# Optimization experiments

Hardware: AMD Instinct MI355X
Metric: run time of the kernel (lower is better)

## Reference

```python
import jax, jax.numpy as jnp
import numpy as np
from jax import lax

H_HID, W_HID = 8, 12
N_PAIR = H_HID * W_HID   # 96
NF = 32                  # mlp_nfilters
C_FEAT = 512 + 2         # phi_im channels + (x,y) coords


def _conv_relu(x, w, b):
    # 3x3 conv, stride 1, SAME padding (SingleConvBlock), then ReLU
    y = lax.conv_general_dilated(x, w, (1, 1), 'SAME',
                                 dimension_numbers=('NCHW', 'OIHW', 'NCHW'))
    return jax.nn.relu(y + b[None, :, None, None])


def _maxpool2(x):
    return lax.reduce_window(x, -jnp.inf, lax.max, (1, 1, 2, 2), (1, 1, 2, 2), 'VALID')


def setup_inputs() -> dict:
    key = jax.random.key(0)
    ks = jax.random.split(key, 16)
    d = {}
    d['x'] = jax.random.normal(ks[0], (4, 3, 64, 96), jnp.float32)
    d['sen_embed'] = jax.random.normal(ks[1], (4, 384), jnp.float32)

    def p(k, shape, fan_in):
        return (jax.random.normal(k, shape, jnp.float32) / np.float32(np.sqrt(fan_in)))

    d['enc1_w'] = p(ks[2], (64, 3, 3, 3), 3 * 9);      d['enc1_b'] = p(ks[3], (64,), 64)
    d['enc2_w'] = p(ks[4], (128, 64, 3, 3), 64 * 9);   d['enc2_b'] = p(ks[5], (128,), 128)
    d['enc3_w'] = p(ks[6], (256, 128, 3, 3), 128 * 9); d['enc3_b'] = p(ks[7], (256,), 256)
    d['enc4_w'] = p(ks[8], (512, 256, 3, 3), 256 * 9); d['enc4_b'] = p(ks[9], (512,), 512)
    d['g1_w'] = p(ks[10], (1412, 256), 1412);          d['g1_b'] = p(ks[11], (256,), 256)
    d['g2_w'] = p(ks[12], (256, 256), 256);            d['g2_b'] = p(ks[13], (256,), 256)
    d['g3_w'] = p(ks[14], (256, N_PAIR * NF), 256);    d['g3_b'] = p(ks[15], (N_PAIR * NF,), N_PAIR * NF)
    return d


def _forward(x, sen_embed, enc1_w, enc1_b, enc2_w, enc2_b, enc3_w, enc3_b,
             enc4_w, enc4_b, g1_w, g1_b, g2_w, g2_b, g3_w, g3_b):
    # ---- conv encoder ----
    e1 = _conv_relu(x, enc1_w, enc1_b)                     # [B,64,64,96]
    e2 = _conv_relu(_maxpool2(e1), enc2_w, enc2_b)         # [B,128,32,48]
    e3 = _conv_relu(_maxpool2(e2), enc3_w, enc3_b)         # [B,256,16,24]
    phi_im = _conv_relu(_maxpool2(e3), enc4_w, enc4_b)     # [B,512,8,12]
    B = phi_im.shape[0]

    # ---- coordinate grid (matches torch.meshgrid default 'ij' then reshape) ----
    xc = jnp.linspace(-1.0, 1.0, W_HID, dtype=phi_im.dtype)
    yc = jnp.linspace(-1.0, 1.0, H_HID, dtype=phi_im.dtype)
    xg, yg = jnp.meshgrid(xc, yc, indexing='ij')           # each [12,8]
    coord = jnp.stack([xg.reshape(H_HID, W_HID), yg.reshape(H_HID, W_HID)], axis=0)
    coord = jnp.broadcast_to(coord[None], (B, 2, H_HID, W_HID))

    # per-location features F: [B, n_pair, 514]
    F = jnp.concatenate([phi_im, coord], axis=1).reshape(B, C_FEAT, N_PAIR).transpose(0, 2, 1)

    # ---- all-pairs relation network ----
    # pair feature at (a,c) = concat(F[c], F[a], sen_embed); exploit linearity of first
    # Linear to avoid materializing the [B,n,n,1412] concat tensor (same math).
    A, Bm, Cm = g1_w[:C_FEAT], g1_w[C_FEAT:2 * C_FEAT], g1_w[2 * C_FEAT:]
    u = F @ A                                # i-part,  [B,n,256]
    v = F @ Bm                               # j-part,  [B,n,256]
    ws = sen_embed @ Cm + g1_b               # sentence part, [B,256]
    h1 = jax.nn.relu(u[:, None, :, :] + v[:, :, None, :] + ws[:, None, None, :])  # [B,n,n,256]
    h2 = jax.nn.relu(h1 @ g2_w + g2_b)                                           # [B,n,n,256]
    out = jax.nn.relu(h2 @ g3_w + g3_b)                                          # [B,n,n,3072]

    # sum over all n_pair^2 pairs, reshape to feature map [B,32,8,12]
    phi = out.sum(axis=(1, 2)).reshape(B, NF, H_HID, W_HID)
    return phi


def reference(x, sen_embed, enc1_w, enc1_b, enc2_w, enc2_b, enc3_w, enc3_b,
              enc4_w, enc4_b, g1_w, g1_b, g2_w, g2_b, g3_w, g3_b):
    return _forward(x, sen_embed, enc1_w, enc1_b, enc2_w, enc2_b, enc3_w, enc3_b,
                    enc4_w, enc4_b, g1_w, g1_b, g2_w, g2_b, g3_w, g3_b)
```

## Files before the change

kernel.cpp:

```cpp
#include <hip/hip_runtime.h>
#include <hip/hip_bf16.h>

using bf16 = __hip_bfloat16;
typedef __attribute__((ext_vector_type(8))) short short8;
typedef __attribute__((ext_vector_type(4))) float f32x4;

static __device__ __forceinline__ bf16 f2b(float x) { return __float2bfloat16(x); }
static __device__ __forceinline__ float b2f(bf16 x) { return __bfloat162float(x); }
static __device__ __forceinline__ short fb(float x) {
  bf16 h = __float2bfloat16(fmaxf(x, 0.f));
  return *(short*)&h;
}

static __device__ __forceinline__ void gload_lds16(const void* g, void* l) {
  auto gp = (const __attribute__((address_space(1))) unsigned int*)g;
  auto lp = (__attribute__((address_space(3))) unsigned int*)l;
  __builtin_amdgcn_global_load_lds(gp, lp, 16, 0, 0);
}

__global__ void conv1_nhwc_kernel(const float* __restrict__ x, const float* __restrict__ w,
                                  const float* __restrict__ bias, bf16* __restrict__ out) {
  const int H = 64, W = 96, HW = H * W;
  __shared__ float wl[27 * 64];
  int tid = threadIdx.x;
  for (int idx = tid; idx < 27 * 64; idx += 256) {
    int k = idx >> 6, oc_ = idx & 63;
    wl[idx] = w[oc_ * 27 + k];
  }
  __syncthreads();
  int oc = tid & 63;
  int pg = blockIdx.x * 4 + (tid >> 6);
  int b = pg / HW, pix = pg - b * HW;
  int y = pix / W, xx0 = pix - y * W;
  float acc = bias[oc];
  #pragma unroll
  for (int ic = 0; ic < 3; ++ic) {
    const float* xp = x + ((size_t)b * 3 + ic) * HW;
    #pragma unroll
    for (int ky = 0; ky < 3; ++ky) {
      int yy = y + ky - 1;
      if (yy < 0 || yy >= H) continue;
      #pragma unroll
      for (int kx = 0; kx < 3; ++kx) {
        int xx = xx0 + kx - 1;
        if (xx < 0 || xx >= W) continue;
        acc += xp[yy * W + xx] * wl[(ic * 9 + ky * 3 + kx) * 64 + oc];
      }
    }
  }
  out[(size_t)pg * 64 + oc] = f2b(fmaxf(acc, 0.f));
}

__global__ void pool_im2col_kernel(const bf16* __restrict__ src, bf16* __restrict__ dst,
                                   int H, int W, int C) {
  int n8 = C >> 3, Hp = H >> 1, Wp = W >> 1;
  int total = 4 * Hp * Wp * 9 * n8;
  int i = blockIdx.x * blockDim.x + threadIdx.x;
  if (i >= total) return;
  int v = i % n8;
  int t = i / n8;
  int tap = t % 9;
  int row = t / 9;
  int HWp = Hp * Wp;
  int b = row / HWp, pix = row - b * HWp;
  int yp = pix / Wp, xp = pix - yp * Wp;
  int yy = yp + tap / 3 - 1, xx = xp + tap % 3 - 1;
  short8 outv = {0, 0, 0, 0, 0, 0, 0, 0};
  if (yy >= 0 && yy < Hp && xx >= 0 && xx < Wp) {
    const short8* s = (const short8*)src;
    size_t base = ((size_t)(b * H + 2 * yy) * W + 2 * xx) * n8 + v;
    short8 a0 = s[base], a1 = s[base + n8];
    short8 a2 = s[base + (size_t)W * n8], a3 = s[base + (size_t)W * n8 + n8];
    #pragma unroll
    for (int e = 0; e < 8; ++e) {
      unsigned short m0 = (unsigned short)a0[e], m1 = (unsigned short)a1[e];
      unsigned short m2 = (unsigned short)a2[e], m3 = (unsigned short)a3[e];
      unsigned short m = m0 > m1 ? m0 : m1;
      unsigned short n = m2 > m3 ? m2 : m3;
      outv[e] = (short)(m > n ? m : n);
    }
  }
  ((short8*)dst)[(size_t)row * (9 * n8) + tap * n8 + v] = outv;
}

__global__ void prep_kernel(const float* __restrict__ w2, const float* __restrict__ w3,
                            const float* __restrict__ w4, const float* __restrict__ g1w,
                            const float* __restrict__ sen, float* __restrict__ outz,
                            bf16* __restrict__ w2r, bf16* __restrict__ w3r,
                            bf16* __restrict__ w4r, bf16* __restrict__ wuv,
                            bf16* __restrict__ Fe) {
  const int S1 = 73728, S2 = S1 + 294912, S3 = S2 + 1179648, S4 = S3 + 442368,
            S5 = S4 + 12288, S6 = S5 + 24576, S7 = S6 + 36864;
  int i = blockIdx.x * 256 + threadIdx.x;
  if (i < S1) {
    int j = i, K = 576, IC = 64;
    int oc = j / K, r = j - oc * K, tap = r / IC, ic = r - tap * IC;
    w2r[j] = f2b(w2[((size_t)oc * IC + ic) * 9 + tap]);
  } else if (i < S2) {
    int j = i - S1, K = 1152, IC = 128;
    int oc = j / K, r = j - oc * K, tap = r / IC, ic = r - tap * IC;
    w3r[j] = f2b(w3[((size_t)oc * IC + ic) * 9 + tap]);
  } else if (i < S3) {
    int j = i - S2, K = 2304, IC = 256;
    int oc = j / K, r = j - oc * K, tap = r / IC, ic = r - tap * IC;
    w4r[j] = f2b(w4[((size_t)oc * IC + ic) * 9 + tap]);
  } else if (i < S4) {
    int j = i - S3;
    int n = j / 576, c = j - n * 576;
    float val = 0.f;
    if (n < 256)      { if (c < 514) val = g1w[(size_t)c * 256 + n]; }
    else if (n < 512) { if (c < 514) val = g1w[(size_t)(514 + c) * 256 + (n - 256)]; }
    else              { if (c < 384) val = g1w[(size_t)(1028 + c) * 256 + (n - 512)]; }
    wuv[j] = f2b(val);
  } else if (i < S5) {
    outz[i - S4] = 0.f;
  } else if (i < S6) {
    int j = i - S5;
    int r = j >> 6, cc = j & 63;
    int p = r % 96;
    float val = 0.f;
    if (cc == 0) val = -1.0f + 2.0f * (float)(p / 8) / 11.0f;
    else if (cc == 1) val = -1.0f + 2.0f * (float)(p % 8) / 7.0f;
    Fe[(size_t)r * 576 + 512 + cc] = f2b(val);
  } else if (i < S7) {
    int j = i - S6;
    int r = j / 576, c = j - r * 576;
    float val = (r < 4 && c < 384) ? sen[r * 384 + c] : 0.f;
    Fe[(size_t)(384 + r) * 576 + c] = f2b(val);
  }
}

__global__ void transpose2_kernel(const float* __restrict__ g2w, const float* __restrict__ g3w,
                                  bf16* __restrict__ w2t, bf16* __restrict__ w3t) {
  __shared__ bf16 t[32][33];
  int bid = blockIdx.x;
  const float* in;
  bf16* out;
  int R, C, c0, r0;
  if (bid < 64) { in = g2w; out = w2t; R = 256; C = 256; c0 = (bid & 7) * 32; r0 = (bid >> 3) * 32; }
  else { int b2 = bid - 64; in = g3w; out = w3t; R = 256; C = 3072; c0 = (b2 % 96) * 32; r0 = (b2 / 96) * 32; }
  int x = threadIdx.x & 31, y = threadIdx.x >> 5;
  for (int yy = y; yy < 32; yy += 8) {
    int r = r0 + yy, c = c0 + x;
    if (r < R && c < C) t[yy][x] = f2b(in[(size_t)r * C + c]);
  }
  __syncthreads();
  for (int yy = y; yy < 32; yy += 8) {
    int c = c0 + yy, r = r0 + x;
    if (r < R && c < C) out[(size_t)c * R + r] = t[x][yy];
  }
}

__launch_bounds__(256)
__global__ void gemm64_kernel(const bf16* __restrict__ A, const bf16* __restrict__ Wt,
                              const float* __restrict__ bias, bf16* __restrict__ outb,
                              float* __restrict__ outf, int K, int ldout, int mode) {
  int m0 = blockIdx.y * 64, n0 = blockIdx.x * 64;
  __shared__ __align__(16) short A_lds[64 * 64];
  __shared__ __align__(16) short B_lds[64 * 64];
  int tid = threadIdx.x, w = tid >> 6, l = tid & 63;
  int quad = l >> 4, l16 = l & 15;
  f32x4 acc[4];
  #pragma unroll
  for (int nt = 0; nt < 4; ++nt)
    #pragma unroll
    for (int e = 0; e < 4; ++e) acc[nt][e] = 0.f;

  int lrow = l >> 3;
  int c_sw = (l & 7) ^ lrow;
  const bf16* ag = A + (size_t)(m0 + w * 16 + lrow) * K + c_sw * 8;
  const bf16* bg = Wt + (size_t)(n0 + w * 16 + lrow) * K + c_sw * 8;
  short* al = A_lds + ((size_t)w * 128 + l) * 8;
  short* bl = B_lds + ((size_t)w * 128 + l) * 8;

  for (int kc = 0; kc < K; kc += 64) {
    if (kc) __syncthreads();
    #pragma unroll
    for (int i = 0; i < 2; ++i) {
      gload_lds16(ag + kc + (size_t)i * 8 * K, al + i * 512);
      gload_lds16(bg + kc + (size_t)i * 8 * K, bl + i * 512);
    }
    __syncthreads();
    #pragma unroll
    for (int ks = 0; ks < 64; ks += 32) {
      int cb = (ks >> 3) + quad;
      int mr = w * 16 + l16;
      short8 af = *(const short8*)&A_lds[mr * 64 + ((cb ^ (mr & 7)) * 8)];
      #pragma unroll
      for (int nt = 0; nt < 4; ++nt) {
        int nr = nt * 16 + l16;
        short8 bf = *(const short8*)&B_lds[nr * 64 + ((cb ^ (nr & 7)) * 8)];
        acc[nt] = __builtin_amdgcn_mfma_f32_16x16x32_bf16(af, bf, acc[nt], 0, 0, 0);
      }
    }
  }
  #pragma unroll
  for (int nt = 0; nt < 4; ++nt) {
    int gcol = n0 + nt * 16 + l16;
    float bv = (mode == 0) ? bias[gcol] : 0.f;
    #pragma unroll
    for (int r = 0; r < 4; ++r) {
      int grow = m0 + w * 16 + quad * 4 + r;
      if (mode == 0) outb[(size_t)grow * ldout + gcol] = f2b(fmaxf(acc[nt][r] + bv, 0.f));
      else           outf[(size_t)grow * ldout + gcol] = acc[nt][r];
    }
  }
}

__launch_bounds__(256)
__global__ void gemm2_kernel(const float* __restrict__ uvws, const float* __restrict__ g1b,
                             const bf16* __restrict__ w2t, const float* __restrict__ g2b,
                             bf16* __restrict__ h2) {
  int b = blockIdx.z;
  int m0 = blockIdx.y * 128;
  int n0 = blockIdx.x * 128;
  __shared__ __align__(16) short A_lds[128 * 64];
  __shared__ __align__(16) short B_lds[128 * 64];
  __shared__ __align__(16) float wsl[256];
  int tid = threadIdx.x, w = tid >> 6, l = tid & 63;
  int quad = l >> 4, l16 = l & 15;
  int mw = (w >> 1) * 64, nw = (w & 1) * 64;
  f32x4 acc[4][4];
  #pragma unroll
  for (int i = 0; i < 4; ++i)
    #pragma unroll
    for (int j = 0; j < 4; ++j)
      #pragma unroll
      for (int e = 0; e < 4; ++e) acc[i][j][e] = 0.f;

  wsl[tid] = uvws[(size_t)(384 + b) * 768 + 512 + tid] + g1b[tid];

  int lrow = l >> 3;
  int c_sw = (l & 7) ^ lrow;
  const bf16* bg = w2t + (size_t)(n0 + w * 32 + lrow) * 256 + c_sw * 8;
  short* bl = B_lds + ((size_t)w * 256 + l) * 8;

  int row = tid >> 1, ks0 = (tid & 1) * 32;
  int m = m0 + row;
  int i_idx = m / 96, j_idx = m - i_idx * 96;
  const float* up = uvws + (size_t)(b * 96 + j_idx) * 768 + ks0;
  const float* vp = uvws + (size_t)(b * 96 + i_idx) * 768 + 256 + ks0;
  __syncthreads();

  for (int kc = 0; kc < 256; kc += 64) {
    if (kc) __syncthreads();
    #pragma unroll
    for (int i = 0; i < 4; ++i)
      gload_lds16(bg + kc + (size_t)i * 8 * 256, bl + i * 512);
    {
      const float4* u4 = (const float4*)(up + kc);
      const float4* v4 = (const float4*)(vp + kc);
      const float4* w4 = (const float4*)&wsl[kc + ks0];
      #pragma unroll
      for (int ch = 0; ch < 4; ++ch) {
        short8 pack;
        #pragma unroll
        for (int q = 0; q < 2; ++q) {
          float4 uu = u4[ch * 2 + q], vv = v4[ch * 2 + q], ww = w4[ch * 2 + q];
          pack[q * 4 + 0] = fb(uu.x + vv.x + ww.x);
          pack[q * 4 + 1] = fb(uu.y + vv.y + ww.y);
          pack[q * 4 + 2] = fb(uu.z + vv.z + ww.z);
          pack[q * 4 + 3] = fb(uu.w + vv.w + ww.w);
        }
        int lc = (ks0 >> 3) + ch;
        *(short8*)&A_lds[row * 64 + ((lc ^ (row & 7)) * 8)] = pack;
      }
    }
    __syncthreads();
    #pragma unroll
    for (int ks = 0; ks < 64; ks += 32) {
      int cb = (ks >> 3) + quad;
      short8 af[4], bfr[4];
      #pragma unroll
      for (int mt = 0; mt < 4; ++mt) {
        int mr = mw + mt * 16 + l16;
        af[mt] = *(const short8*)&A_lds[mr * 64 + ((cb ^ (mr & 7)) * 8)];
      }
      #pragma unroll
      for (int nt = 0; nt < 4; ++nt) {
        int nr = nw + nt * 16 + l16;
        bfr[nt] = *(const short8*)&B_lds[nr * 64 + ((cb ^ (nr & 7)) * 8)];
      }
      #pragma unroll
      for (int mt = 0; mt < 4; ++mt)
        #pragma unroll
        for (int nt = 0; nt < 4; ++nt)
          acc[mt][nt] = __builtin_amdgcn_mfma_f32_16x16x32_bf16(af[mt], bfr[nt], acc[mt][nt], 0, 0, 0);
    }
  }
  bf16* h2b = h2 + (size_t)b * 9216 * 256;
  #pragma unroll
  for (int nt = 0; nt < 4; ++nt) {
    int gcol = n0 + nw + nt * 16 + l16;
    float bias = g2b[gcol];
    #pragma unroll
    for (int mt = 0; mt < 4; ++mt) {
      #pragma unroll
      for (int r = 0; r < 4; ++r) {
        int grow = m0 + mw + mt * 16 + quad * 4 + r;
        h2b[(size_t)grow * 256 + gcol] = f2b(fmaxf(acc[mt][nt][r] + bias, 0.f));
      }
    }
  }
}

__launch_bounds__(256)
__global__ void gemm3_kernel(const bf16* __restrict__ h2, const bf16* __restrict__ w3t,
                             const float* __restrict__ g3b, float* __restrict__ phi) {
  int g = blockIdx.x;
  int x = g & 7, s = g >> 3;
  int grp = s / 24;
  int nIdx = s - grp * 24;
  int mb = grp * 8 + x;
  int b = mb / 72;
  int m0 = (mb - b * 72) * 128;
  int n0 = nIdx * 128;
  __shared__ __align__(16) short A_lds[128 * 64];
  __shared__ __align__(16) short B_lds[128 * 64];
  int tid = threadIdx.x, w = tid >> 6, l = tid & 63;
  int quad = l >> 4, l16 = l & 15;
  int mw = (w >> 1) * 64, nw = (w & 1) * 64;
  f32x4 acc[4][4];
  #pragma unroll
  for (int i = 0; i < 4; ++i)
    #pragma unroll
    for (int j = 0; j < 4; ++j)
      #pragma unroll
      for (int e = 0; e < 4; ++e) acc[i][j][e] = 0.f;

  const int K = 256;
  int lrow = l >> 3;
  int c_sw = (l & 7) ^ lrow;
  const bf16* ag = h2 + (size_t)(b * 9216 + m0 + w * 32 + lrow) * K + c_sw * 8;
  const bf16* bg = w3t + (size_t)(n0 + w * 32 + lrow) * K + c_sw * 8;
  short* al = A_lds + ((size_t)w * 256 + l) * 8;
  short* bl = B_lds + ((size_t)w * 256 + l) * 8;

  for (int kc = 0; kc < K; kc += 64) {
    if (kc) __syncthreads();
    #pragma unroll
    for (int i = 0; i < 4; ++i) {
      gload_lds16(ag + kc + (size_t)i * 8 * K, al + i * 512);
      gload_lds16(bg + kc + (size_t)i * 8 * K, bl + i * 512);
    }
    __syncthreads();
    #pragma unroll
    for (int ks = 0; ks < 64; ks += 32) {
      int cb = (ks >> 3) + quad;
      short8 af[4], bfr[4];
      #pragma unroll
      for (int mt = 0; mt < 4; ++mt) {
        int mr = mw + mt * 16 + l16;
        af[mt] = *(const short8*)&A_lds[mr * 64 + ((cb ^ (mr & 7)) * 8)];
      }
      #pragma unroll
      for (int nt = 0; nt < 4; ++nt) {
        int nr = nw + nt * 16 + l16;
        bfr[nt] = *(const short8*)&B_lds[nr * 64 + ((cb ^ (nr & 7)) * 8)];
      }
      #pragma unroll
      for (int mt = 0; mt < 4; ++mt)
        #pragma unroll
        for (int nt = 0; nt < 4; ++nt)
          acc[mt][nt] = __builtin_amdgcn_mfma_f32_16x16x32_bf16(af[mt], bfr[nt], acc[mt][nt], 0, 0, 0);
    }
  }
  #pragma unroll
  for (int nt = 0; nt < 4; ++nt) {
    int gcol = n0 + nw + nt * 16 + l16;
    float bias = g3b[gcol];
    float s2 = 0.f;
    #pragma unroll
    for (int mt = 0; mt < 4; ++mt)
      #pragma unroll
      for (int r = 0; r < 4; ++r)
        s2 += fmaxf(acc[mt][nt][r] + bias, 0.f);
    s2 += __shfl_xor(s2, 16, 64);
    s2 += __shfl_xor(s2, 32, 64);
    if (quad == 0) atomicAdd(&phi[b * 3072 + gcol], s2);
  }
}

extern "C" void kernel_launch(void* const* d_in, const int* in_sizes, int n_in,
                              void* d_out, int out_size, void* d_ws, size_t ws_size,
                              hipStream_t stream) {
  const float* x   = (const float*)d_in[0];
  const float* sen = (const float*)d_in[1];
  const float* w1  = (const float*)d_in[2];
  const float* b1  = (const float*)d_in[3];
  const float* w2  = (const float*)d_in[4];
  const float* b2  = (const float*)d_in[5];
  const float* w3  = (const float*)d_in[6];
  const float* b3  = (const float*)d_in[7];
  const float* w4  = (const float*)d_in[8];
  const float* b4  = (const float*)d_in[9];
  const float* g1w = (const float*)d_in[10];
  const float* g1b = (const float*)d_in[11];
  const float* g2w = (const float*)d_in[12];
  const float* g2b = (const float*)d_in[13];
  const float* g3w = (const float*)d_in[14];
  const float* g3b = (const float*)d_in[15];
  float* out = (float*)d_out;

  char* wsp = (char*)d_ws;
  size_t off = 0;
  auto alloc = [&](size_t bytes) {
    char* p = wsp + off;
    off += (bytes + 255) & ~(size_t)255;
    return (void*)p;
  };
  bf16* e1   = (bf16*)alloc((size_t)4 * 6144 * 64 * 2);
  bf16* col2 = (bf16*)alloc((size_t)6144 * 576 * 2);
  bf16* e2   = (bf16*)alloc((size_t)6144 * 128 * 2);
  bf16* col3 = (bf16*)alloc((size_t)1536 * 1152 * 2);
  bf16* e3   = (bf16*)alloc((size_t)1536 * 256 * 2);
  bf16* col4 = (bf16*)alloc((size_t)384 * 2304 * 2);
  bf16* Fe   = (bf16*)alloc((size_t)448 * 576 * 2);
  bf16* wuv  = (bf16*)alloc((size_t)768 * 576 * 2);
  float* uvws = (float*)alloc((size_t)448 * 768 * 4);
  bf16* w2r  = (bf16*)alloc((size_t)128 * 576 * 2);
  bf16* w3r  = (bf16*)alloc((size_t)256 * 1152 * 2);
  bf16* w4r  = (bf16*)alloc((size_t)512 * 2304 * 2);
  bf16* w2t  = (bf16*)alloc((size_t)256 * 256 * 2);
  bf16* w3t  = (bf16*)alloc((size_t)3072 * 256 * 2);
  bf16* h2   = (bf16*)alloc((size_t)4 * 9216 * 256 * 2);

  prep_kernel<<<dim3(8064), 256, 0, stream>>>(w2, w3, w4, g1w, sen, out, w2r, w3r, w4r, wuv, Fe);
  transpose2_kernel<<<dim3(832), 256, 0, stream>>>(g2w, g3w, w2t, w3t);

  conv1_nhwc_kernel<<<dim3(6144), 256, 0, stream>>>(x, w1, b1, e1);
  pool_im2col_kernel<<<dim3(1728), 256, 0, stream>>>(e1, col2, 64, 96, 64);
  gemm64_kernel<<<dim3(2, 96), 256, 0, stream>>>(col2, w2r, b2, e2, nullptr, 576, 128, 0);
  pool_im2col_kernel<<<dim3(864), 256, 0, stream>>>(e2, col3, 32, 48, 128);
  gemm64_kernel<<<dim3(4, 24), 256, 0, stream>>>(col3, w3r, b3, e3, nullptr, 1152, 256, 0);
  pool_im2col_kernel<<<dim3(432), 256, 0, stream>>>(e3, col4, 16, 24, 256);
  gemm64_kernel<<<dim3(8, 6), 256, 0, stream>>>(col4, w4r, b4, Fe, nullptr, 2304, 576, 0);

  gemm64_kernel<<<dim3(12, 7), 256, 0, stream>>>(Fe, wuv, nullptr, nullptr, uvws, 576, 768, 2);
  gemm2_kernel<<<dim3(2, 72, 4), 256, 0, stream>>>(uvws, g1b, w2t, g2b, h2);
  gemm3_kernel<<<dim3(6912), 256, 0, stream>>>(h2, w3t, g3b, out);
}
```

Baseline: 283.1 us.

## Fuse maxpool into conv epilogues and use implicit-GEMM im2col loads

Conv1 now computes the four pre-pool outputs per pooled pixel and writes only the pooled tensor. Conv2 and conv3 reorder GEMM rows so that each pool window falls in one MFMA quad and max-pool in the epilogue. All GEMM convs gather im2col rows directly from the pooled NHWC input, with a zero buffer for padding. This removes three pool_im2col kernels and the large col/e intermediates, at the cost of irregular gather addresses in the GEMM A-load.

```diff
diff --git a/kernel.cpp b/kernel.cpp
--- a/kernel.cpp
+++ b/kernel.cpp
@@ -18,8 +18,8 @@
   __builtin_amdgcn_global_load_lds(gp, lp, 16, 0, 0);
 }
 
-__global__ void conv1_nhwc_kernel(const float* __restrict__ x, const float* __restrict__ w,
-                                  const float* __restrict__ bias, bf16* __restrict__ out) {
+__global__ void conv1pool_kernel(const float* __restrict__ x, const float* __restrict__ w,
+                                 const float* __restrict__ bias, bf16* __restrict__ out) {
   const int H = 64, W = 96, HW = H * W;
   __shared__ float wl[27 * 64];
   int tid = threadIdx.x;
@@ -29,58 +29,40 @@
   }
   __syncthreads();
   int oc = tid & 63;
-  int pg = blockIdx.x * 4 + (tid >> 6);
-  int b = pg / HW, pix = pg - b * HW;
-  int y = pix / W, xx0 = pix - y * W;
-  float acc = bias[oc];
+  int pp = blockIdx.x * 4 + (tid >> 6);
+  int b = pp / 1536, rem = pp - b * 1536;
+  int yp = rem / 48, xp = rem - yp * 48;
+  int y0 = 2 * yp - 1, x0 = 2 * xp - 1;
+  float win[3][4][4];
   #pragma unroll
   for (int ic = 0; ic < 3; ++ic) {
-    const float* xp = x + ((size_t)b * 3 + ic) * HW;
-    #pragma unroll
-    for (int ky = 0; ky < 3; ++ky) {
-      int yy = y + ky - 1;
-      if (yy < 0 || yy >= H) continue;
-      #pragma unroll
-      for (int kx = 0; kx < 3; ++kx) {
-        int xx = xx0 + kx - 1;
-        if (xx < 0 || xx >= W) continue;
-        acc += xp[yy * W + xx] * wl[(ic * 9 + ky * 3 + kx) * 64 + oc];
-      }
-    }
-  }
-  out[(size_t)pg * 64 + oc] = f2b(fmaxf(acc, 0.f));
-}
-
-__global__ void pool_im2col_kernel(const bf16* __restrict__ src, bf16* __restrict__ dst,
-                                   int H, int W, int C) {
-  int n8 = C >> 3, Hp = H >> 1, Wp = W >> 1;
-  int total = 4 * Hp * Wp * 9 * n8;
-  int i = blockIdx.x * blockDim.x + threadIdx.x;
-  if (i >= total) return;
-  int v = i % n8;
-  int t = i / n8;
-  int tap = t % 9;
-  int row = t / 9;
-  int HWp = Hp * Wp;
-  int b = row / HWp, pix = row - b * HWp;
-  int yp = pix / Wp, xp = pix - yp * Wp;
-  int yy = yp + tap / 3 - 1, xx = xp + tap % 3 - 1;
-  short8 outv = {0, 0, 0, 0, 0, 0, 0, 0};
-  if (yy >= 0 && yy < Hp && xx >= 0 && xx < Wp) {
-    const short8* s = (const short8*)src;
-    size_t base = ((size_t)(b * H + 2 * yy) * W + 2 * xx) * n8 + v;
-    short8 a0 = s[base], a1 = s[base + n8];
-    short8 a2 = s[base + (size_t)W * n8], a3 = s[base + (size_t)W * n8 + n8];
-    #pragma unroll
-    for (int e = 0; e < 8; ++e) {
-      unsigned short m0 = (unsigned short)a0[e], m1 = (unsigned short)a1[e];
-      unsigned short m2 = (unsigned short)a2[e], m3 = (unsigned short)a3[e];
-      unsigned short m = m0 > m1 ? m0 : m1;
-      unsigned short n = m2 > m3 ? m2 : m3;
-      outv[e] = (short)(m > n ? m : n);
-    }
-  }
-  ((short8*)dst)[(size_t)row * (9 * n8) + tap * n8 + v] = outv;
+    const float* xsrc = x + ((size_t)b * 3 + ic) * HW;
+    #pragma unroll
+    for (int dy = 0; dy < 4; ++dy) {
+      int yy = y0 + dy;
+      #pragma unroll
+      for (int dx = 0; dx < 4; ++dx) {
+        int xx = x0 + dx;
+        win[ic][dy][dx] = (yy >= 0 && yy < H && xx >= 0 && xx < W) ? xsrc[yy * W + xx] : 0.f;
+      }
+    }
+  }
+  float cmax = -1e30f;
+  #pragma unroll
+  for (int sy = 0; sy < 2; ++sy)
+    #pragma unroll
+    for (int sx = 0; sx < 2; ++sx) {
+      float acc = 0.f;
+      #pragma unroll
+      for (int ic = 0; ic < 3; ++ic)
+        #pragma unroll
+        for (int ky = 0; ky < 3; ++ky)
+          #pragma unroll
+          for (int kx = 0; kx < 3; ++kx)
+            acc += win[ic][sy + ky][sx + kx] * wl[(ic * 9 + ky * 3 + kx) * 64 + oc];
+      cmax = fmaxf(cmax, acc);
+    }
+  out[(size_t)pp * 64 + oc] = f2b(fmaxf(cmax + bias[oc], 0.f));
 }
 
 __global__ void prep_kernel(const float* __restrict__ w2, const float* __restrict__ w3,
@@ -88,9 +70,9 @@
                             const float* __restrict__ sen, float* __restrict__ outz,
                             bf16* __restrict__ w2r, bf16* __restrict__ w3r,
                             bf16* __restrict__ w4r, bf16* __restrict__ wuv,
-                            bf16* __restrict__ Fe) {
+                            bf16* __restrict__ Fe, float* __restrict__ zb) {
   const int S1 = 73728, S2 = S1 + 294912, S3 = S2 + 1179648, S4 = S3 + 442368,
-            S5 = S4 + 12288, S6 = S5 + 24576, S7 = S6 + 36864;
+            S5 = S4 + 12288, S6 = S5 + 24576, S7 = S6 + 36864, S8 = S7 + 64;
   int i = blockIdx.x * 256 + threadIdx.x;
   if (i < S1) {
     int j = i, K = 576, IC = 64;
@@ -127,6 +109,8 @@
     int r = j / 576, c = j - r * 576;
     float val = (r < 4 && c < 384) ? sen[r * 384 + c] : 0.f;
     Fe[(size_t)(384 + r) * 576 + c] = f2b(val);
+  } else if (i < S8) {
+    zb[i - S7] = 0.f;
   }
 }
 
@@ -151,10 +135,14 @@
   }
 }
 
+template <int CBITS, bool POOL>
 __launch_bounds__(256)
-__global__ void gemm64_kernel(const bf16* __restrict__ A, const bf16* __restrict__ Wt,
-                              const float* __restrict__ bias, bf16* __restrict__ outb,
-                              float* __restrict__ outf, int K, int ldout, int mode) {
+__global__ void gemm_conv_kernel(const bf16* __restrict__ pin, const bf16* __restrict__ Wt,
+                                 const float* __restrict__ bias, bf16* __restrict__ outb,
+                                 const bf16* __restrict__ zbuf,
+                                 int Hi, int Wi, int N, int ldout) {
+  const int C = 1 << CBITS;
+  const int K = 9 << CBITS;
   int m0 = blockIdx.y * 64, n0 = blockIdx.x * 64;
   __shared__ __align__(16) short A_lds[64 * 64];
   __shared__ __align__(16) short B_lds[64 * 64];
@@ -168,6 +156,94 @@
 
   int lrow = l >> 3;
   int c_sw = (l & 7) ^ lrow;
+  int ybase[2], xbase[2], bidx[2];
+  #pragma unroll
+  for (int i = 0; i < 2; ++i) {
+    int row = m0 + w * 16 + i * 8 + lrow;
+    if (POOL) {
+      int pg = row >> 2, sub = row & 3;
+      int Wh = Wi >> 1, HW2 = (Hi >> 1) * Wh;
+      int b = pg / HW2, rem = pg - b * HW2;
+      int py = rem / Wh, px = rem - py * Wh;
+      bidx[i] = b; ybase[i] = 2 * py + (sub >> 1); xbase[i] = 2 * px + (sub & 1);
+    } else {
+      int HW = Hi * Wi;
+      int b = row / HW, pix = row - b * HW;
+      int yy = pix / Wi;
+      bidx[i] = b; ybase[i] = yy; xbase[i] = pix - yy * Wi;
+    }
+  }
+  const bf16* bg = Wt + (size_t)(n0 + w * 16 + lrow) * K + c_sw * 8;
+  short* al = A_lds + ((size_t)w * 128 + l) * 8;
+  short* bl = B_lds + ((size_t)w * 128 + l) * 8;
+
+  for (int kc = 0; kc < K; kc += 64) {
+    if (kc) __syncthreads();
+    int colt = kc + c_sw * 8;
+    int tap = colt >> CBITS, cc = colt & (C - 1);
+    int ty = tap / 3, tx = tap - 3 * ty;
+    #pragma unroll
+    for (int i = 0; i < 2; ++i) {
+      int yy = ybase[i] + ty - 1, xx = xbase[i] + tx - 1;
+      const bf16* asrc = (yy >= 0 && yy < Hi && xx >= 0 && xx < Wi)
+          ? pin + ((((size_t)(bidx[i] * Hi + yy)) * Wi + xx) << CBITS) + cc
+          : zbuf;
+      gload_lds16(asrc, al + i * 512);
+      gload_lds16(bg + kc + (size_t)i * 8 * K, bl + i * 512);
+    }
+    __syncthreads();
+    #pragma unroll
+    for (int ks = 0; ks < 64; ks += 32) {
+      int cb = (ks >> 3) + quad;
+      int mr = w * 16 + l16;
+      short8 af = *(const short8*)&A_lds[mr * 64 + ((cb ^ (mr & 7)) * 8)];
+      #pragma unroll
+      for (int nt = 0; nt < 4; ++nt) {
+        int nr = nt * 16 + l16;
+        short8 bf = *(const short8*)&B_lds[nr * 64 + ((cb ^ (nr & 7)) * 8)];
+        acc[nt] = __builtin_amdgcn_mfma_f32_16x16x32_bf16(af, bf, acc[nt], 0, 0, 0);
+      }
+    }
+  }
+  if (POOL) {
+    int pg = (m0 + w * 16 + quad * 4) >> 2;
+    #pragma unroll
+    for (int nt = 0; nt < 4; ++nt) {
+      int gcol = n0 + nt * 16 + l16;
+      float bv = bias[gcol];
+      float m = fmaxf(fmaxf(acc[nt][0], acc[nt][1]), fmaxf(acc[nt][2], acc[nt][3]));
+      outb[(size_t)pg * N + gcol] = f2b(fmaxf(m + bv, 0.f));
+    }
+  } else {
+    #pragma unroll
+    for (int nt = 0; nt < 4; ++nt) {
+      int gcol = n0 + nt * 16 + l16;
+      float bv = bias[gcol];
+      #pragma unroll
+      for (int r = 0; r < 4; ++r) {
+        int grow = m0 + w * 16 + quad * 4 + r;
+        outb[(size_t)grow * ldout + gcol] = f2b(fmaxf(acc[nt][r] + bv, 0.f));
+      }
+    }
+  }
+}
+
+__launch_bounds__(256)
+__global__ void gemm64_kernel(const bf16* __restrict__ A, const bf16* __restrict__ Wt,
+                              float* __restrict__ outf, int K, int ldout) {
+  int m0 = blockIdx.y * 64, n0 = blockIdx.x * 64;
+  __shared__ __align__(16) short A_lds[64 * 64];
+  __shared__ __align__(16) short B_lds[64 * 64];
+  int tid = threadIdx.x, w = tid >> 6, l = tid & 63;
+  int quad = l >> 4, l16 = l & 15;
+  f32x4 acc[4];
+  #pragma unroll
+  for (int nt = 0; nt < 4; ++nt)
+    #pragma unroll
+    for (int e = 0; e < 4; ++e) acc[nt][e] = 0.f;
+
+  int lrow = l >> 3;
+  int c_sw = (l & 7) ^ lrow;
   const bf16* ag = A + (size_t)(m0 + w * 16 + lrow) * K + c_sw * 8;
   const bf16* bg = Wt + (size_t)(n0 + w * 16 + lrow) * K + c_sw * 8;
   short* al = A_lds + ((size_t)w * 128 + l) * 8;
@@ -197,12 +273,10 @@
   #pragma unroll
   for (int nt = 0; nt < 4; ++nt) {
     int gcol = n0 + nt * 16 + l16;
-    float bv = (mode == 0) ? bias[gcol] : 0.f;
     #pragma unroll
     for (int r = 0; r < 4; ++r) {
       int grow = m0 + w * 16 + quad * 4 + r;
-      if (mode == 0) outb[(size_t)grow * ldout + gcol] = f2b(fmaxf(acc[nt][r] + bv, 0.f));
-      else           outf[(size_t)grow * ldout + gcol] = acc[nt][r];
+      outf[(size_t)grow * ldout + gcol] = acc[nt][r];
     }
   }
 }
@@ -409,12 +483,9 @@
     off += (bytes + 255) & ~(size_t)255;
     return (void*)p;
   };
-  bf16* e1   = (bf16*)alloc((size_t)4 * 6144 * 64 * 2);
-  bf16* col2 = (bf16*)alloc((size_t)6144 * 576 * 2);
-  bf16* e2   = (bf16*)alloc((size_t)6144 * 128 * 2);
-  bf16* col3 = (bf16*)alloc((size_t)1536 * 1152 * 2);
-  bf16* e3   = (bf16*)alloc((size_t)1536 * 256 * 2);
-  bf16* col4 = (bf16*)alloc((size_t)384 * 2304 * 2);
+  bf16* p1   = (bf16*)alloc((size_t)6144 * 64 * 2);
+  bf16* p2   = (bf16*)alloc((size_t)1536 * 128 * 2);
+  bf16* p3   = (bf16*)alloc((size_t)384 * 256 * 2);
   bf16* Fe   = (bf16*)alloc((size_t)448 * 576 * 2);
   bf16* wuv  = (bf16*)alloc((size_t)768 * 576 * 2);
   float* uvws = (float*)alloc((size_t)448 * 768 * 4);
@@ -424,19 +495,17 @@
   bf16* w2t  = (bf16*)alloc((size_t)256 * 256 * 2);
   bf16* w3t  = (bf16*)alloc((size_t)3072 * 256 * 2);
   bf16* h2   = (bf16*)alloc((size_t)4 * 9216 * 256 * 2);
-
-  prep_kernel<<<dim3(8064), 256, 0, stream>>>(w2, w3, w4, g1w, sen, out, w2r, w3r, w4r, wuv, Fe);
+  float* zbuf = (float*)alloc((size_t)256);
+
+  prep_kernel<<<dim3(8065), 256, 0, stream>>>(w2, w3, w4, g1w, sen, out, w2r, w3r, w4r, wuv, Fe, zbuf);
   transpose2_kernel<<<dim3(832), 256, 0, stream>>>(g2w, g3w, w2t, w3t);
 
-  conv1_nhwc_kernel<<<dim3(6144), 256, 0, stream>>>(x, w1, b1, e1);
-  pool_im2col_kernel<<<dim3(1728), 256, 0, stream>>>(e1, col2, 64, 96, 64);
-  gemm64_kernel<<<dim3(2, 96), 256, 0, stream>>>(col2, w2r, b2, e2, nullptr, 576, 128, 0);
-  pool_im2col_kernel<<<dim3(864), 256, 0, stream>>>(e2, col3, 32, 48, 128);
-  gemm64_kernel<<<dim3(4, 24), 256, 0, stream>>>(col3, w3r, b3, e3, nullptr, 1152, 256, 0);
-  pool_im2col_kernel<<<dim3(432), 256, 0, stream>>>(e3, col4, 16, 24, 256);
-  gemm64_kernel<<<dim3(8, 6), 256, 0, stream>>>(col4, w4r, b4, Fe, nullptr, 2304, 576, 0);
-
-  gemm64_kernel<<<dim3(12, 7), 256, 0, stream>>>(Fe, wuv, nullptr, nullptr, uvws, 576, 768, 2);
+  conv1pool_kernel<<<dim3(1536), 256, 0, stream>>>(x, w1, b1, p1);
+  gemm_conv_kernel<6, true><<<dim3(2, 96), 256, 0, stream>>>(p1, w2r, b2, p2, (const bf16*)zbuf, 32, 48, 128, 128);
+  gemm_conv_kernel<7, true><<<dim3(4, 24), 256, 0, stream>>>(p2, w3r, b3, p3, (const bf16*)zbuf, 16, 24, 256, 256);
+  gemm_conv_kernel<8, false><<<dim3(8, 6), 256, 0, stream>>>(p3, w4r, b4, Fe, (const bf16*)zbuf, 8, 12, 512, 576);
+
+  gemm64_kernel<<<dim3(12, 7), 256, 0, stream>>>(Fe, wuv, uvws, 576, 768);
   gemm2_kernel<<<dim3(2, 72, 4), 256, 0, stream>>>(uvws, g1b, w2t, g2b, h2);
   gemm3_kernel<<<dim3(6912), 256, 0, stream>>>(h2, w3t, g3b, out);
 }
```

Measured after the change: 248.1 us. 12.4% less time.
